# Kernel tuning notes

Hardware: AMD Instinct MI355X
Metric: run time of the kernel (lower is better)

Reference implementation:

```python
import jax, jax.numpy as jnp
import numpy as np

N = 100000      # nodes
E = 3200000     # edges (avg degree 32)
D_IN = 128      # input feature dim
H = 16          # hidden_size = GCN in/out channels
M = 16          # memory_size
SLOPE = 0.01    # F.leaky_relu default negative slope


def setup_inputs() -> dict:
    key = jax.random.key(0)
    ks = jax.random.split(key, 24)
    def p(i, shape):
        return jax.random.normal(ks[i], shape, dtype=jnp.float32) * 0.05
    return {
        "x": jax.random.normal(ks[0], (N, D_IN), dtype=jnp.float32),
        "edge_index": jax.random.randint(ks[1], (2, E), 0, N),
        # preprocess Linears (torch Linear: y = x @ W.T + b)
        "W1": p(2, (256, D_IN)), "b1": p(3, (256,)),
        "W2": p(4, (H, 256)),    "b2": p(5, (H,)),
        # EvolveGNN_O layer 1: memory buffer (zeros), GRU, weight_transform, GCN bias
        "mem1": jnp.zeros((M,), jnp.float32),
        "g1_Wih": p(6, (3 * M, M)), "g1_Whh": p(7, (3 * M, M)),
        "g1_bih": p(8, (3 * M,)),   "g1_bhh": p(9, (3 * M,)),
        "wt1_W": p(10, (H * H, M)), "wt1_b": p(11, (H * H,)),
        "gcn1_b": p(12, (H,)),
        # EvolveGNN_O layer 2
        "mem2": jnp.zeros((M,), jnp.float32),
        "g2_Wih": p(13, (3 * M, M)), "g2_Whh": p(14, (3 * M, M)),
        "g2_bih": p(15, (3 * M,)),   "g2_bhh": p(16, (3 * M,)),
        "wt2_W": p(17, (H * H, M)), "wt2_b": p(18, (H * H,)),
        "gcn2_b": p(19, (H,)),
        # postprocessing Linear(hidden, 2)
        "Wout": p(20, (2, H)), "bout": p(21, (2,)),
    }


def _leaky(x):
    return jnp.where(x >= 0, x, SLOPE * x)


def _gru_step(x, Wih, Whh, bih, bhh):
    # PyTorch nn.GRU single step, h0 = 0 (default when h not provided)
    h = jnp.zeros_like(x)
    gi = Wih @ x + bih
    gh = Whh @ h + bhh
    ir, iz, inn = jnp.split(gi, 3)
    hr, hz, hn = jnp.split(gh, 3)
    r = jax.nn.sigmoid(ir + hr)
    z = jax.nn.sigmoid(iz + hz)
    n = jnp.tanh(inn + r * hn)
    return (1.0 - z) * n + z * h


def _gcn(h, row, col, W, bias):
    # PyG GCNConv: linear transform, symmetric gcn_norm (self-loops already
    # appended to row/col), gather from row, scatter-add to col, add bias.
    n = h.shape[0]
    xl = h @ W.T                                          # [N, H]
    ones = jnp.ones(row.shape[0], h.dtype)
    deg = jax.ops.segment_sum(ones, col, num_segments=n)  # in-degree incl. self-loop
    dis = jnp.where(deg > 0, jax.lax.rsqrt(deg), 0.0)
    norm = dis[row] * dis[col]                            # [E + N]
    out = jax.ops.segment_sum(xl[row] * norm[:, None], col, num_segments=n)
    return out + bias


def _evolve_gcn(h, row, col, mem, Wih, Whh, bih, bhh, wtW, wtb, gcn_b):
    new_mem = _gru_step(mem, Wih, Whh, bih, bhh)          # GRU-updated memory
    Wnew = (wtW @ new_mem + wtb).reshape(H, H)            # regenerated lin.weight [out, in]
    return _gcn(h, row, col, Wnew, gcn_b)


def reference(x, edge_index, W1, b1, W2, b2,
              mem1, g1_Wih, g1_Whh, g1_bih, g1_bhh, wt1_W, wt1_b, gcn1_b,
              mem2, g2_Wih, g2_Whh, g2_bih, g2_bhh, wt2_W, wt2_b, gcn2_b,
              Wout, bout):
    n = x.shape[0]
    loops = jnp.arange(n, dtype=edge_index.dtype)
    row = jnp.concatenate([edge_index[0], loops])         # sources (+ self-loops)
    col = jnp.concatenate([edge_index[1], loops])         # targets (+ self-loops)

    h = _leaky(x @ W1.T + b1)                             # [N, 256]
    h = _leaky(h @ W2.T + b2)                             # [N, 16]
    h = _leaky(_evolve_gcn(h, row, col, mem1, g1_Wih, g1_Whh, g1_bih, g1_bhh, wt1_W, wt1_b, gcn1_b))
    h = _leaky(_evolve_gcn(h, row, col, mem2, g2_Wih, g2_Whh, g2_bih, g2_bhh, wt2_W, wt2_b, gcn2_b))
    h = h @ Wout.T + bout                                 # [N, 2]
    return jnp.sum(h, axis=-1)                            # [N]
```

## Files before the change

### kernel.cpp

```cpp
#include <hip/hip_runtime.h>
#include <math.h>

#define SLOPE 0.01f
#define BKS   256
#define BSH2  8
#define NBKMAX 512
#define BCAP  10240

typedef short  bf16x8 __attribute__((ext_vector_type(8)));
typedef float  f32x4  __attribute__((ext_vector_type(4)));

__device__ __forceinline__ float lrelu(float v) { return v >= 0.f ? v : SLOPE * v; }

__device__ __forceinline__ unsigned short f2bf(float v) {
    unsigned u = __float_as_uint(v);
    return (unsigned short)((u + 0x7FFFu + ((u >> 16) & 1u)) >> 16);
}
__device__ __forceinline__ float bf2f(unsigned short b) {
    return __uint_as_float(((unsigned)b) << 16);
}

__global__ void prep_k(const float* __restrict__ m1, const float* __restrict__ Wih1,
                       const float* __restrict__ bih1, const float* __restrict__ bhh1,
                       const float* __restrict__ m2, const float* __restrict__ Wih2,
                       const float* __restrict__ bih2, const float* __restrict__ bhh2,
                       const float* __restrict__ wtW1, const float* __restrict__ wtb1,
                       const float* __restrict__ wtW2, const float* __restrict__ wtb2,
                       const float* __restrict__ Wout, const float* __restrict__ bout,
                       const float* __restrict__ W2,
                       float* __restrict__ Wn1, float* __restrict__ Wn2,
                       float* __restrict__ wsum, float* __restrict__ bsum,
                       unsigned short* __restrict__ W2bh, unsigned short* __restrict__ W2bl,
                       int* __restrict__ bfill, int NBK) {
    __shared__ float nm[32];
    int t = threadIdx.x;
    if (t < 32) {
        int L = t >> 4, j = t & 15;
        const float* m   = L ? m2   : m1;
        const float* Wih = L ? Wih2 : Wih1;
        const float* bih = L ? bih2 : bih1;
        const float* bhh = L ? bhh2 : bhh1;
        float gr = bih[j], gz = bih[16 + j], gn = bih[32 + j];
        for (int k = 0; k < 16; ++k) {
            float mk = m[k];
            gr += Wih[j * 16 + k] * mk;
            gz += Wih[(16 + j) * 16 + k] * mk;
            gn += Wih[(32 + j) * 16 + k] * mk;
        }
        float r = 1.f / (1.f + expf(-(gr + bhh[j])));
        float z = 1.f / (1.f + expf(-(gz + bhh[16 + j])));
        float n = tanhf(gn + r * bhh[32 + j]);
        nm[t] = (1.f - z) * n;
    }
    __syncthreads();
    float s1 = wtb1[t], s2 = wtb2[t];
    for (int k = 0; k < 16; ++k) {
        s1 += wtW1[t * 16 + k] * nm[k];
        s2 += wtW2[t * 16 + k] * nm[16 + k];
    }
    Wn1[t] = s1;
    Wn2[t] = s2;
    for (int i = t; i < 4096; i += 256) {
        float v = W2[i];
        unsigned short h = f2bf(v);
        W2bh[i] = h;
        W2bl[i] = f2bf(v - bf2f(h));
    }
    if (t < 16) wsum[t] = Wout[t] + Wout[16 + t];
    if (t == 0) bsum[0] = bout[0] + bout[1];
    for (int i = t; i < NBK; i += 256) bfill[i] = i * BCAP;
}

__global__ void wsplit_k(const float* __restrict__ W1,
                         unsigned short* __restrict__ W1h,
                         unsigned short* __restrict__ W1l) {
    int i = blockIdx.x * 256 + threadIdx.x;
    float v = W1[i];
    unsigned short h = f2bf(v);
    W1h[i] = h;
    W1l[i] = f2bf(v - bf2f(h));
}

__global__ void bscat_k(const int* __restrict__ row, const int* __restrict__ col,
                        int* __restrict__ bfill, int2* __restrict__ stage,
                        int E, int NBK) {
    __shared__ int lcnt[NBKMAX];
    __shared__ int lbase[NBKMAX];
    int t = threadIdx.x;
    for (int i = t; i < NBK; i += 256) lcnt[i] = 0;
    __syncthreads();
    int base = blockIdx.x * 4096;
    int r[16], d[16], sl[16];
#pragma unroll
    for (int i = 0; i < 16; ++i) {
        int e = base + i * 256 + t;
        if (e < E) {
            r[i]  = row[e];
            d[i]  = col[e];
            sl[i] = atomicAdd(&lcnt[d[i] >> BSH2], 1);
        } else d[i] = -1;
    }
    __syncthreads();
    for (int i = t; i < NBK; i += 256)
        lbase[i] = lcnt[i] ? atomicAdd(bfill + i, lcnt[i]) : 0;
    __syncthreads();
#pragma unroll
    for (int i = 0; i < 16; ++i) {
        if (d[i] >= 0)
            stage[lbase[d[i] >> BSH2] + sl[i]] = make_int2(r[i], d[i]);
    }
}

__global__ __launch_bounds__(512) void cscan_k(const int* __restrict__ bfill,
                                               int* __restrict__ bbase2,
                                               int* __restrict__ off,
                                               int NBK, int N, int E) {
    __shared__ int s[512];
    int t = threadIdx.x;
    int v = (t < NBK) ? (bfill[t] - t * BCAP) : 0;
    s[t] = v;
    __syncthreads();
    for (int d = 1; d < 512; d <<= 1) {
        int u = (t >= d) ? s[t - d] : 0;
        __syncthreads();
        s[t] += u;
        __syncthreads();
    }
    if (t < NBK) bbase2[t] = s[t] - v;
    if (t == 0) { bbase2[NBK] = E; off[N] = E; }
}

__global__ void bproc_k(const int2* __restrict__ stage, const int* __restrict__ bbase2,
                        int* __restrict__ off, float* __restrict__ dis,
                        int* __restrict__ srcs, int N) {
    __shared__ int lh[BKS];
    __shared__ int ssc[BKS];
    const int b  = blockIdx.x;
    const int t  = threadIdx.x;
    const int sb = b * BCAP;
    const int e0 = bbase2[b];
    const int cnt = bbase2[b + 1] - e0;
    lh[t] = 0;
    __syncthreads();
    for (int i = t; i < cnt; i += 256) {
        int2 v = stage[sb + i];
        atomicAdd(&lh[v.y & (BKS - 1)], 1);
    }
    __syncthreads();
    int c = lh[t];
    ssc[t] = c;
    __syncthreads();
    for (int d = 1; d < 256; d <<= 1) {
        int u = (t >= d) ? ssc[t - d] : 0;
        __syncthreads();
        ssc[t] += u;
        __syncthreads();
    }
    int ex = ssc[t] - c;
    {
        int node = b * BKS + t;
        if (node < N) {
            off[node] = e0 + ex;
            dis[node] = rsqrtf((float)(c + 1));
        }
    }
    __syncthreads();
    lh[t] = ex;
    __syncthreads();
    for (int i = t; i < cnt; i += 256) {
        int2 w = stage[sb + i];
        int pos = e0 + atomicAdd(&lh[w.y & (BKS - 1)], 1);
        srcs[pos] = w.x;
    }
}

__global__ __launch_bounds__(512, 4) void mlp_k(
        const float* __restrict__ x,
        const unsigned short* __restrict__ W1h,
        const unsigned short* __restrict__ W1l,
        const float* __restrict__ b1,
        const unsigned short* __restrict__ W2bh,
        const unsigned short* __restrict__ W2bl,
        const float* __restrict__ b2,
        const float* __restrict__ Wn1,
        const float* __restrict__ dis,
        unsigned short* __restrict__ xl, int N) {
    __shared__ float sbuf[11008];
    unsigned short* xh  = (unsigned short*)sbuf;
    unsigned short* xlo = xh + 8704;
    unsigned short* h1h = (unsigned short*)sbuf;
    float*          h2p = sbuf + 8448;

    const int t      = threadIdx.x;
    const int nl     = t & 63;
    const int q      = __builtin_amdgcn_readfirstlane(t >> 6);
    const int lane15 = t & 15;
    const int quad   = (t & 63) >> 4;
    const int node   = blockIdx.x * 64 + nl;
    const bool valid = node < N;

    {
        const float4* x4 = (const float4*)x;
        const size_t tb = (size_t)blockIdx.x * 2048;
        unsigned* xh32 = (unsigned*)xh;
        unsigned* xl32 = (unsigned*)xlo;
#pragma unroll
        for (int kk = 0; kk < 4; ++kk) {
            int idx  = kk * 512 + t;
            int row  = idx >> 5;
            int col4 = idx & 31;
            float4 v = make_float4(0.f, 0.f, 0.f, 0.f);
            if (blockIdx.x * 64 + row < N) v = x4[tb + idx];
            unsigned short hx = f2bf(v.x), hy = f2bf(v.y);
            unsigned short hz = f2bf(v.z), hw = f2bf(v.w);
            unsigned short lx = f2bf(v.x - bf2f(hx)), ly = f2bf(v.y - bf2f(hy));
            unsigned short lz = f2bf(v.z - bf2f(hz)), lw = f2bf(v.w - bf2f(hw));
            int base = row * 68 + col4 * 2;
            *(uint2*)(xh32 + base) =
                make_uint2((unsigned)hx | ((unsigned)hy << 16),
                           (unsigned)hz | ((unsigned)hw << 16));
            *(uint2*)(xl32 + base) =
                make_uint2((unsigned)lx | ((unsigned)ly << 16),
                           (unsigned)lz | ((unsigned)lw << 16));
        }
    }
    __syncthreads();

    f32x4 acc[4][2];
#pragma unroll
    for (int mt = 0; mt < 4; ++mt)
#pragma unroll
        for (int nt = 0; nt < 2; ++nt)
            acc[mt][nt] = (f32x4){0.f, 0.f, 0.f, 0.f};

#pragma unroll
    for (int nt = 0; nt < 2; ++nt) {
        bf16x8 bh[4], bl[4];
#pragma unroll
        for (int ks = 0; ks < 4; ++ks) {
            size_t wo = (size_t)(q * 32 + nt * 16 + lane15) * 128 + ks * 32 + quad * 8;
            bh[ks] = *(const bf16x8*)(W1h + wo);
            bl[ks] = *(const bf16x8*)(W1l + wo);
        }
#pragma unroll
        for (int ks = 0; ks < 4; ++ks) {
            const int koff = ks * 32 + quad * 8;
#pragma unroll
            for (int mt = 0; mt < 4; ++mt) {
                bf16x8 ah = *(const bf16x8*)(xh  + (16 * mt + lane15) * 136 + koff);
                bf16x8 al = *(const bf16x8*)(xlo + (16 * mt + lane15) * 136 + koff);
                acc[mt][nt] = __builtin_amdgcn_mfma_f32_16x16x32_bf16(ah, bh[ks], acc[mt][nt], 0, 0, 0);
                acc[mt][nt] = __builtin_amdgcn_mfma_f32_16x16x32_bf16(ah, bl[ks], acc[mt][nt], 0, 0, 0);
                acc[mt][nt] = __builtin_amdgcn_mfma_f32_16x16x32_bf16(al, bh[ks], acc[mt][nt], 0, 0, 0);
            }
        }
    }
    __syncthreads();

    const int kh  = q >> 2;
    const int mt2 = q & 3;
    bf16x8 w2hf[4], w2lf[4];
#pragma unroll
    for (int ks2 = 0; ks2 < 4; ++ks2) {
        int wo = lane15 * 256 + (kh * 4 + ks2) * 32 + quad * 8;
        w2hf[ks2] = *(const bf16x8*)(W2bh + wo);
        w2lf[ks2] = *(const bf16x8*)(W2bl + wo);
    }

#pragma unroll
    for (int nt = 0; nt < 2; ++nt) {
        int hu = q * 32 + nt * 16 + lane15;
        float bb = b1[hu];
#pragma unroll
        for (int mt = 0; mt < 4; ++mt) {
            int row0 = 16 * mt + quad * 4;
#pragma unroll
            for (int r = 0; r < 4; ++r) {
                float v = lrelu(acc[mt][nt][r] + bb);
                h1h[(row0 + r) * 264 + hu] = f2bf(v);
            }
        }
    }
    __syncthreads();

    f32x4 a2 = (f32x4){0.f, 0.f, 0.f, 0.f};
#pragma unroll
    for (int ks2 = 0; ks2 < 4; ++ks2) {
        const int koff = (kh * 4 + ks2) * 32 + quad * 8;
        bf16x8 ah = *(const bf16x8*)(h1h + (16 * mt2 + lane15) * 264 + koff);
        a2 = __builtin_amdgcn_mfma_f32_16x16x32_bf16(ah, w2hf[ks2], a2, 0, 0, 0);
        a2 = __builtin_amdgcn_mfma_f32_16x16x32_bf16(ah, w2lf[ks2], a2, 0, 0, 0);
    }
    {
        float* dst = h2p + kh * 1280 + (16 * mt2 + quad * 4) * 20 + lane15;
        dst[0] = a2[0]; dst[20] = a2[1]; dst[40] = a2[2]; dst[60] = a2[3];
    }
    __syncthreads();

    {
        const f32x4* pa = (const f32x4*)(h2p + nl * 20);
        const f32x4* pb = (const f32x4*)(h2p + 1280 + nl * 20);
        f32x4 s[4];
#pragma unroll
        for (int i = 0; i < 4; ++i) s[i] = pa[i] + pb[i];
        float o0 = 0.f, o1 = 0.f;
        const float* wr0 = Wn1 + (2 * q) * 16;
        const float* wr1 = Wn1 + (2 * q + 1) * 16;
#pragma unroll
        for (int j = 0; j < 16; ++j) {
            float h = lrelu(s[j >> 2][j & 3] + b2[j]);
            o0 = fmaf(wr0[j], h, o0);
            o1 = fmaf(wr1[j], h, o1);
        }
        if (valid) {
            float d = dis[node];
            unsigned pk = (unsigned)f2bf(d * o0) | ((unsigned)f2bf(d * o1) << 16);
            *(unsigned*)(xl + (size_t)node * 16 + 2 * q) = pk;
        }
    }
}

__global__ void gather1_k(const int* __restrict__ off, const int* __restrict__ srcs,
                          const float* __restrict__ dis,
                          const unsigned short* __restrict__ xin,
                          const float* __restrict__ bias, const float* __restrict__ Wn2,
                          unsigned short* __restrict__ xout, int N) {
    __shared__ float w[256];
    {
        int j = threadIdx.x >> 4, c = threadIdx.x & 15;
        w[threadIdx.x] = Wn2[c * 16 + j];
    }
    __syncthreads();
    int g = blockIdx.x * 16 + (threadIdx.x >> 4);
    int c = threadIdx.x & 15;
    if (g >= N) return;
    float acc = bf2f(xin[(size_t)g * 16 + c]);
    int e  = off[g];
    int e1 = off[g + 1];
    for (; e + 7 < e1; e += 8) {
        int s0 = srcs[e],     s1 = srcs[e + 1], s2 = srcs[e + 2], s3 = srcs[e + 3];
        int s4 = srcs[e + 4], s5 = srcs[e + 5], s6 = srcs[e + 6], s7 = srcs[e + 7];
        float v0 = bf2f(xin[(size_t)s0 * 16 + c]);
        float v1 = bf2f(xin[(size_t)s1 * 16 + c]);
        float v2 = bf2f(xin[(size_t)s2 * 16 + c]);
        float v3 = bf2f(xin[(size_t)s3 * 16 + c]);
        float v4 = bf2f(xin[(size_t)s4 * 16 + c]);
        float v5 = bf2f(xin[(size_t)s5 * 16 + c]);
        float v6 = bf2f(xin[(size_t)s6 * 16 + c]);
        float v7 = bf2f(xin[(size_t)s7 * 16 + c]);
        acc += ((v0 + v1) + (v2 + v3)) + ((v4 + v5) + (v6 + v7));
    }
    for (; e < e1; ++e)
        acc += bf2f(xin[(size_t)srcs[e] * 16 + c]);
    float d = dis[g];
    float h = lrelu(fmaf(d, acc, bias[c]));
    float o = 0.f;
#pragma unroll
    for (int j = 0; j < 16; ++j) o = fmaf(w[j * 16 + c], __shfl(h, j, 16), o);
    xout[(size_t)g * 16 + c] = f2bf(d * o);
}

__global__ void gather2_k(const int* __restrict__ off, const int* __restrict__ srcs,
                          const float* __restrict__ dis,
                          const unsigned short* __restrict__ xin,
                          const float* __restrict__ bias, const float* __restrict__ wsum,
                          const float* __restrict__ bsum, float* __restrict__ out, int N) {
    int g = blockIdx.x * 16 + (threadIdx.x >> 4);
    int c = threadIdx.x & 15;
    if (g >= N) return;
    float acc = bf2f(xin[(size_t)g * 16 + c]);
    int e  = off[g];
    int e1 = off[g + 1];
    for (; e + 7 < e1; e += 8) {
        int s0 = srcs[e],     s1 = srcs[e + 1], s2 = srcs[e + 2], s3 = srcs[e + 3];
        int s4 = srcs[e + 4], s5 = srcs[e + 5], s6 = srcs[e + 6], s7 = srcs[e + 7];
        float v0 = bf2f(xin[(size_t)s0 * 16 + c]);
        float v1 = bf2f(xin[(size_t)s1 * 16 + c]);
        float v2 = bf2f(xin[(size_t)s2 * 16 + c]);
        float v3 = bf2f(xin[(size_t)s3 * 16 + c]);
        float v4 = bf2f(xin[(size_t)s4 * 16 + c]);
        float v5 = bf2f(xin[(size_t)s5 * 16 + c]);
        float v6 = bf2f(xin[(size_t)s6 * 16 + c]);
        float v7 = bf2f(xin[(size_t)s7 * 16 + c]);
        acc += ((v0 + v1) + (v2 + v3)) + ((v4 + v5) + (v6 + v7));
    }
    for (; e < e1; ++e)
        acc += bf2f(xin[(size_t)srcs[e] * 16 + c]);
    float v = wsum[c] * lrelu(fmaf(dis[g], acc, bias[c]));
#pragma unroll
    for (int m = 1; m < 16; m <<= 1) v += __shfl_xor(v, m);
    if (c == 0) out[g] = v + bsum[0];
}

extern "C" void kernel_launch(void* const* d_in, const int* in_sizes, int n_in,
                              void* d_out, int out_size, void* d_ws, size_t ws_size,
                              hipStream_t stream) {
    const float* x      = (const float*)d_in[0];
    const int*   edge   = (const int*)d_in[1];
    const float* W1     = (const float*)d_in[2];
    const float* b1     = (const float*)d_in[3];
    const float* W2     = (const float*)d_in[4];
    const float* b2     = (const float*)d_in[5];
    const float* mem1   = (const float*)d_in[6];
    const float* g1_Wih = (const float*)d_in[7];
    const float* g1_bih = (const float*)d_in[9];
    const float* g1_bhh = (const float*)d_in[10];
    const float* wt1_W  = (const float*)d_in[11];
    const float* wt1_b  = (const float*)d_in[12];
    const float* gcn1_b = (const float*)d_in[13];
    const float* mem2   = (const float*)d_in[14];
    const float* g2_Wih = (const float*)d_in[15];
    const float* g2_bih = (const float*)d_in[17];
    const float* g2_bhh = (const float*)d_in[18];
    const float* wt2_W  = (const float*)d_in[19];
    const float* wt2_b  = (const float*)d_in[20];
    const float* gcn2_b = (const float*)d_in[21];
    const float* Wout   = (const float*)d_in[22];
    const float* bout   = (const float*)d_in[23];
    float* out = (float*)d_out;

    const int N = in_sizes[0] / 128;
    const int E = in_sizes[1] / 2;
    const int* row = edge;
    const int* col = edge + E;

    const int NBK = (N + BKS - 1) >> BSH2;
    const int gM  = (N + 63) / 64;
    const int gG  = (N + 15) / 16;
    const int gB  = (E + 4095) / 4096;

    float* ws    = (float*)d_ws;
    float* bufA  = ws;
    float* bufB  = bufA + (size_t)N * 16;
    float* dis   = bufB + (size_t)N * 16;
    float* sm    = dis + N;
    float* Wn1   = sm;
    float* Wn2   = sm + 256;
    float* wsum  = sm + 512;
    float* bsum  = sm + 528;
    unsigned short* W2bh = (unsigned short*)(sm + 544);
    unsigned short* W2bl = (unsigned short*)(sm + 2592);
    unsigned short* W1h = (unsigned short*)(sm + 4640);
    unsigned short* W1l = (unsigned short*)(sm + 21024);
    int*   bfill = (int*)(sm + 37408);
    int*   bbase2= bfill + NBKMAX;
    int*   off   = bbase2 + NBKMAX + 1;
    int*   srcs  = off + N + 1;
    size_t stoff = (size_t)(srcs + E - (int*)d_ws);
    stoff = (stoff + 3) & ~(size_t)3;
    int2*  stage = (int2*)((int*)d_ws + stoff);

    prep_k<<<1, 256, 0, stream>>>(mem1, g1_Wih, g1_bih, g1_bhh,
                                  mem2, g2_Wih, g2_bih, g2_bhh,
                                  wt1_W, wt1_b, wt2_W, wt2_b,
                                  Wout, bout, W2, Wn1, Wn2, wsum, bsum,
                                  W2bh, W2bl, bfill, NBK);
    wsplit_k<<<128, 256, 0, stream>>>(W1, W1h, W1l);
    bscat_k<<<gB, 256, 0, stream>>>(row, col, bfill, stage, E, NBK);
    cscan_k<<<1, 512, 0, stream>>>(bfill, bbase2, off, NBK, N, E);
    bproc_k<<<NBK, 256, 0, stream>>>(stage, bbase2, off, dis, srcs, N);
    mlp_k<<<gM, 512, 0, stream>>>(x, W1h, W1l, b1, W2bh, W2bl, b2, Wn1, dis,
                                  (unsigned short*)bufA, N);
    gather1_k<<<gG, 256, 0, stream>>>(off, srcs, dis, (unsigned short*)bufA,
                                      gcn1_b, Wn2, (unsigned short*)bufB, N);
    gather2_k<<<gG, 256, 0, stream>>>(off, srcs, dis, (unsigned short*)bufB,
                                      gcn2_b, wsum, bsum, out, N);
}
```

Before: 329.6 us.

## Pack staged edges to 32 bits and coalesce bucket scatter via LDS

The bucket-scatter kernel now sorts each block's edges by bucket in shared memory (using a prefix scan over bucket counts), then writes them to the staging buffer in contiguous runs instead of scattered per-thread stores. Staged edges are packed into one 32-bit word (source<<8 | low 8 bits of destination) rather than an int2, halving staging traffic. The bucket-processing kernel runs with 512 threads and unrolls its loads four at a time. The packing assumes source indices fit in 24 bits, and the extra LDS and scan add per-block overhead.

```diff
diff --git a/kernel.cpp b/kernel.cpp
--- a/kernel.cpp
+++ b/kernel.cpp
@@ -81,13 +81,18 @@
     W1l[i] = f2bf(v - bf2f(h));
 }
 
-__global__ void bscat_k(const int* __restrict__ row, const int* __restrict__ col,
-                        int* __restrict__ bfill, int2* __restrict__ stage,
-                        int E, int NBK) {
+__global__ __launch_bounds__(256) void bscat_k(
+        const int* __restrict__ row, const int* __restrict__ col,
+        int* __restrict__ bfill, unsigned* __restrict__ stage,
+        int E, int NBK) {
     __shared__ int lcnt[NBKMAX];
+    __shared__ int s[NBKMAX];
     __shared__ int lbase[NBKMAX];
+    __shared__ unsigned ledge[4096];
+    __shared__ unsigned short lbkt[4096];
     int t = threadIdx.x;
     for (int i = t; i < NBK; i += 256) lcnt[i] = 0;
+    for (int j = t; j < 4096; j += 256) lbkt[j] = 0xFFFFu;
     __syncthreads();
     int base = blockIdx.x * 4096;
     int r[16], d[16], sl[16];
@@ -101,13 +106,34 @@
         } else d[i] = -1;
     }
     __syncthreads();
+    s[t]       = (t < NBK)       ? lcnt[t]       : 0;
+    s[t + 256] = (t + 256 < NBK) ? lcnt[t + 256] : 0;
+    __syncthreads();
+    for (int dd = 1; dd < NBKMAX; dd <<= 1) {
+        int u0 = (t >= dd)       ? s[t - dd]       : 0;
+        int u1 = (t + 256 >= dd) ? s[t + 256 - dd] : 0;
+        __syncthreads();
+        s[t]       += u0;
+        s[t + 256] += u1;
+        __syncthreads();
+    }
     for (int i = t; i < NBK; i += 256)
         lbase[i] = lcnt[i] ? atomicAdd(bfill + i, lcnt[i]) : 0;
     __syncthreads();
 #pragma unroll
     for (int i = 0; i < 16; ++i) {
-        if (d[i] >= 0)
-            stage[lbase[d[i] >> BSH2] + sl[i]] = make_int2(r[i], d[i]);
+        if (d[i] >= 0) {
+            int bkt = d[i] >> BSH2;
+            int idx = (s[bkt] - lcnt[bkt]) + sl[i];
+            ledge[idx] = ((unsigned)r[i] << 8) | (unsigned)(d[i] & (BKS - 1));
+            lbkt[idx]  = (unsigned short)bkt;
+        }
+    }
+    __syncthreads();
+    for (int j = t; j < 4096; j += 256) {
+        int bkt = lbkt[j];
+        if (bkt != 0xFFFF)
+            stage[lbase[bkt] + (j - (s[bkt] - lcnt[bkt]))] = ledge[j];
     }
 }
 
@@ -130,9 +156,10 @@
     if (t == 0) { bbase2[NBK] = E; off[N] = E; }
 }
 
-__global__ void bproc_k(const int2* __restrict__ stage, const int* __restrict__ bbase2,
-                        int* __restrict__ off, float* __restrict__ dis,
-                        int* __restrict__ srcs, int N) {
+__global__ __launch_bounds__(512) void bproc_k(
+        const unsigned* __restrict__ stage, const int* __restrict__ bbase2,
+        int* __restrict__ off, float* __restrict__ dis,
+        int* __restrict__ srcs, int N) {
     __shared__ int lh[BKS];
     __shared__ int ssc[BKS];
     const int b  = blockIdx.x;
@@ -140,37 +167,64 @@
     const int sb = b * BCAP;
     const int e0 = bbase2[b];
     const int cnt = bbase2[b + 1] - e0;
-    lh[t] = 0;
-    __syncthreads();
-    for (int i = t; i < cnt; i += 256) {
-        int2 v = stage[sb + i];
-        atomicAdd(&lh[v.y & (BKS - 1)], 1);
-    }
-    __syncthreads();
-    int c = lh[t];
-    ssc[t] = c;
-    __syncthreads();
-    for (int d = 1; d < 256; d <<= 1) {
-        int u = (t >= d) ? ssc[t - d] : 0;
+    if (t < BKS) lh[t] = 0;
+    __syncthreads();
+    {
+        int i = t;
+        for (; i + 1536 < cnt; i += 2048) {
+            unsigned v0 = stage[sb + i];
+            unsigned v1 = stage[sb + i + 512];
+            unsigned v2 = stage[sb + i + 1024];
+            unsigned v3 = stage[sb + i + 1536];
+            atomicAdd(&lh[v0 & (BKS - 1)], 1);
+            atomicAdd(&lh[v1 & (BKS - 1)], 1);
+            atomicAdd(&lh[v2 & (BKS - 1)], 1);
+            atomicAdd(&lh[v3 & (BKS - 1)], 1);
+        }
+        for (; i < cnt; i += 512)
+            atomicAdd(&lh[stage[sb + i] & (BKS - 1)], 1);
+    }
+    __syncthreads();
+    int c = (t < BKS) ? lh[t] : 0;
+    if (t < BKS) ssc[t] = c;
+    __syncthreads();
+    for (int d = 1; d < BKS; d <<= 1) {
+        int u = (t >= d && t < BKS) ? ssc[t - d] : 0;
         __syncthreads();
-        ssc[t] += u;
+        if (t < BKS) ssc[t] += u;
         __syncthreads();
     }
-    int ex = ssc[t] - c;
-    {
+    if (t < BKS) {
+        int ex = ssc[t] - c;
         int node = b * BKS + t;
         if (node < N) {
             off[node] = e0 + ex;
             dis[node] = rsqrtf((float)(c + 1));
         }
-    }
-    __syncthreads();
-    lh[t] = ex;
-    __syncthreads();
-    for (int i = t; i < cnt; i += 256) {
-        int2 w = stage[sb + i];
-        int pos = e0 + atomicAdd(&lh[w.y & (BKS - 1)], 1);
-        srcs[pos] = w.x;
+        lh[t] = ex;
+    }
+    __syncthreads();
+    {
+        int i = t;
+        for (; i + 1536 < cnt; i += 2048) {
+            unsigned v0 = stage[sb + i];
+            unsigned v1 = stage[sb + i + 512];
+            unsigned v2 = stage[sb + i + 1024];
+            unsigned v3 = stage[sb + i + 1536];
+            int p0 = e0 + atomicAdd(&lh[v0 & (BKS - 1)], 1);
+            int p1 = e0 + atomicAdd(&lh[v1 & (BKS - 1)], 1);
+            int p2 = e0 + atomicAdd(&lh[v2 & (BKS - 1)], 1);
+            int p3 = e0 + atomicAdd(&lh[v3 & (BKS - 1)], 1);
+            srcs[p0] = (int)(v0 >> 8);
+            srcs[p1] = (int)(v1 >> 8);
+            srcs[p2] = (int)(v2 >> 8);
+            srcs[p3] = (int)(v3 >> 8);
+        }
+        for (; i < cnt; i += 512) {
+            unsigned v = stage[sb + i];
+            int pos = e0 + atomicAdd(&lh[v & (BKS - 1)], 1);
+            srcs[pos] = (int)(v >> 8);
+        }
     }
 }
 
@@ -448,7 +502,7 @@
     int*   srcs  = off + N + 1;
     size_t stoff = (size_t)(srcs + E - (int*)d_ws);
     stoff = (stoff + 3) & ~(size_t)3;
-    int2*  stage = (int2*)((int*)d_ws + stoff);
+    unsigned* stage = (unsigned*)((int*)d_ws + stoff);
 
     prep_k<<<1, 256, 0, stream>>>(mem1, g1_Wih, g1_bih, g1_bhh,
                                   mem2, g2_Wih, g2_bih, g2_bhh,
@@ -458,7 +512,7 @@
     wsplit_k<<<128, 256, 0, stream>>>(W1, W1h, W1l);
     bscat_k<<<gB, 256, 0, stream>>>(row, col, bfill, stage, E, NBK);
     cscan_k<<<1, 512, 0, stream>>>(bfill, bbase2, off, NBK, N, E);
-    bproc_k<<<NBK, 256, 0, stream>>>(stage, bbase2, off, dis, srcs, N);
+    bproc_k<<<NBK, 512, 0, stream>>>(stage, bbase2, off, dis, srcs, N);
     mlp_k<<<gM, 512, 0, stream>>>(x, W1h, W1l, b1, W2bh, W2bl, b2, Wn1, dis,
                                   (unsigned short*)bufA, N);
     gather1_k<<<gG, 256, 0, stream>>>(off, srcs, dis, (unsigned short*)bufA,
```

Measured after the change: 311.0 us. 5.6% less time.
